# Kernel optimization log

Measured on AMD Instinct MI355X. Metric: run time of the kernel, lower is better.

The kernel has to match this reference:

```python
import jax, jax.numpy as jnp
import numpy as np

N_HEAD = 32
N_KV_HEAD = 8
HEAD_DIM = 64
ROPE_THETA = 10000.0


def apply_rope(x):
    # x: [B, H, T, D], interleaved-pair RoPE (rotary_embedding_torch style)
    B, H, T, D = x.shape
    inv_freq = 1.0 / (ROPE_THETA ** (jnp.arange(0, D, 2, dtype=jnp.float32) / D))  # [D/2]
    ang = jnp.arange(T, dtype=jnp.float32)[:, None] * inv_freq[None, :]  # [T, D/2]
    cos = jnp.cos(ang)[None, None].astype(x.dtype)  # [1,1,T,D/2]
    sin = jnp.sin(ang)[None, None].astype(x.dtype)
    xe = x[..., 0::2]
    xo = x[..., 1::2]
    re = xe * cos - xo * sin
    ro = xo * cos + xe * sin
    return jnp.stack([re, ro], axis=-1).reshape(B, H, T, D)


def setup_inputs() -> dict:
    key = jax.random.key(0)
    ks = jax.random.split(key, 5)
    B, T, C = 2, 2048, 2048
    kv_dim = N_KV_HEAD * HEAD_DIM
    s = 0.02
    return {
        "x": jax.random.normal(ks[0], (B, T, C), jnp.float32),
        "wq": jax.random.normal(ks[1], (C, C), jnp.float32) * s,
        "wk": jax.random.normal(ks[2], (C, kv_dim), jnp.float32) * s,
        "wv": jax.random.normal(ks[3], (C, kv_dim), jnp.float32) * s,
        "wo": jax.random.normal(ks[4], (C, C), jnp.float32) * s,
    }


def reference(x, wq, wk, wv, wo):
    B, T, C = x.shape
    hd = HEAD_DIM
    q = (x @ wq).reshape(B, T, N_HEAD, hd).transpose(0, 2, 1, 3)      # [B,H,T,d]
    k = (x @ wk).reshape(B, T, N_KV_HEAD, hd).transpose(0, 2, 1, 3)   # [B,Hkv,T,d]
    v = (x @ wv).reshape(B, T, N_KV_HEAD, hd).transpose(0, 2, 1, 3)
    q = apply_rope(q)
    k = apply_rope(k)
    rep = N_HEAD // N_KV_HEAD
    k = jnp.repeat(k, rep, axis=1)  # repeat_interleave over head dim
    v = jnp.repeat(v, rep, axis=1)
    att = jnp.einsum('bhqd,bhkd->bhqk', q, k) * (1.0 / np.sqrt(hd))
    causal = jnp.tril(jnp.ones((T, T), dtype=bool))
    att = jnp.where(causal[None, None], att, jnp.finfo(att.dtype).min)
    att = jax.nn.softmax(att, axis=-1)
    y = jnp.einsum('bhqk,bhkd->bhqd', att, v)
    y = y.transpose(0, 2, 1, 3).reshape(B, T, C)
    return y @ wo
```

## Files before the change

kernel.cpp:

```cpp
#include <hip/hip_runtime.h>
#include <hip/hip_bf16.h>
#include <cstdint>
#include <cstddef>


using bf16 = __hip_bfloat16;
using f32x4  = __attribute__((ext_vector_type(4))) float;
using f32x16 = __attribute__((ext_vector_type(16))) float;
using short8 = __attribute__((ext_vector_type(8))) short;
using u32x4  = __attribute__((ext_vector_type(4))) unsigned int;

typedef __attribute__((address_space(1))) const void* gp1_t;
typedef __attribute__((address_space(3))) void*       lp3_t;

#define GLOAD_LDS16(g, l)                                                     \
  __builtin_amdgcn_global_load_lds((gp1_t)(const void*)(g), (lp3_t)(void*)(l), 16, 0, 0)

#define MFMA16(a, b, c) __builtin_amdgcn_mfma_f32_16x16x32_bf16(a, b, c, 0, 0, 0)
#define MFMA32(a, b, c) __builtin_amdgcn_mfma_f32_32x32x16_bf16(a, b, c, 0, 0, 0)

static constexpr int Bd  = 2;
static constexpr int Td  = 2048;
static constexpr int Cd  = 2048;
static constexpr int NH  = 32;
static constexpr int NKV = 8;
static constexpr int HD  = 64;
static constexpr int Md  = Bd * Td;

__device__ inline float bf2f(unsigned short u) {
  union { unsigned int i; float f; } v; v.i = ((unsigned int)u) << 16; return v.f;
}
__device__ inline unsigned short f2bfbits(float f) {
  union { float f; unsigned int u; } v; v.f = f;
  unsigned int r = v.u + 0x7fffu + ((v.u >> 16) & 1u);
  return (unsigned short)(r >> 16);
}
__device__ inline unsigned int pkbf(float a, float b) {
  unsigned int r;
  asm("v_cvt_pk_bf16_f32 %0, %1, %2" : "=v"(r) : "v"(a), "v"(b));
  return r;
}
__device__ inline void plswapf(float& a, float& b) {
  asm("v_permlane32_swap_b32 %0, %1" : "+v"(a), "+v"(b));
}
__device__ inline void plswapu(unsigned int& a, unsigned int& b) {
  asm("v_permlane32_swap_b32 %0, %1" : "+v"(a), "+v"(b));
}
__device__ inline float hmax16(const f32x16& v) {
  float a0 = fmaxf(v[0], v[1]),   a1 = fmaxf(v[2], v[3]);
  float a2 = fmaxf(v[4], v[5]),   a3 = fmaxf(v[6], v[7]);
  float a4 = fmaxf(v[8], v[9]),   a5 = fmaxf(v[10], v[11]);
  float a6 = fmaxf(v[12], v[13]), a7 = fmaxf(v[14], v[15]);
  float b0 = fmaxf(a0, a1), b1 = fmaxf(a2, a3);
  float b2 = fmaxf(a4, a5), b3 = fmaxf(a6, a7);
  return fmaxf(fmaxf(b0, b1), fmaxf(b2, b3));
}
__device__ inline float hsum16(const f32x16& v) {
  float a0 = v[0]+v[1],   a1 = v[2]+v[3],   a2 = v[4]+v[5],   a3 = v[6]+v[7];
  float a4 = v[8]+v[9],   a5 = v[10]+v[11], a6 = v[12]+v[13], a7 = v[14]+v[15];
  float b0 = a0+a1, b1 = a2+a3, b2 = a4+a5, b3 = a6+a7;
  return (b0+b1)+(b2+b3);
}

__global__ __launch_bounds__(256) void prep1_kernel(const float* __restrict__ x,
                                                    const float* __restrict__ wq,
                                                    const float* __restrict__ wk,
                                                    const float* __restrict__ wv,
                                                    bf16* __restrict__ xb,
                                                    bf16* __restrict__ w1) {
  __shared__ float tile[32][33];
  int bid = blockIdx.x, tid = threadIdx.x;
  if (bid < 8192) {
    int i = bid * 256 + tid;
    float4 v = ((const float4*)x)[i];
    ushort4 o;
    o.x = f2bfbits(v.x); o.y = f2bfbits(v.y); o.z = f2bfbits(v.z); o.w = f2bfbits(v.w);
    ((ushort4*)xb)[i] = o;
    return;
  }
  const float* in; bf16* out; int Cc, bx, by;
  if (bid < 12288)      { int l = bid - 8192;  in = wq; out = w1;                        Cc = 2048; bx = l & 63; by = l >> 6; }
  else if (bid < 13312) { int l = bid - 12288; in = wk; out = w1 + (size_t)2048 * 2048;  Cc = 512;  bx = l & 15; by = l >> 4; }
  else                  { int l = bid - 13312; in = wv; out = w1 + (size_t)2560 * 2048;  Cc = 512;  bx = l & 15; by = l >> 4; }
  int tx = tid & 31, ty = tid >> 5;
  int col = bx * 32 + tx;
#pragma unroll
  for (int i = 0; i < 4; ++i) {
    int row = by * 32 + ty + i * 8;
    tile[ty + i * 8][tx] = in[(size_t)row * Cc + col];
  }
  __syncthreads();
#pragma unroll
  for (int i = 0; i < 4; ++i) {
    int orow = bx * 32 + ty + i * 8;
    int ocol = by * 32 + tx;
    out[(size_t)orow * 2048 + ocol] = __float2bfloat16(tile[tx][ty + i * 8]);
  }
}

__global__ __launch_bounds__(256) void transpose_f2b(const float* __restrict__ in,
                                                     bf16* __restrict__ out,
                                                     int R, int Cc) {
  __shared__ float tile[32][33];
  int tx = threadIdx.x & 31, ty = threadIdx.x >> 5;
  int bx = blockIdx.x, by = blockIdx.y;
  int col = bx * 32 + tx;
#pragma unroll
  for (int i = 0; i < 4; ++i) {
    int row = by * 32 + ty + i * 8;
    tile[ty + i * 8][tx] = in[(size_t)row * Cc + col];
  }
  __syncthreads();
#pragma unroll
  for (int i = 0; i < 4; ++i) {
    int orow = bx * 32 + ty + i * 8;
    int ocol = by * 32 + tx;
    out[(size_t)orow * R + ocol] = __float2bfloat16(tile[tx][ty + i * 8]);
  }
}

__global__ __launch_bounds__(512, 2) void gemm_qkv(const bf16* __restrict__ A,
                                                   const bf16* __restrict__ Bt,
                                                   void* __restrict__ Cp,
                                                   int M, int N, int K) {
  __shared__ __align__(16) char lds[114688];
  int tid = threadIdx.x;
  int w = tid >> 6, lane = tid & 63;
  int lr = lane & 15, lg = lane >> 4;
  int m0 = blockIdx.x * 256, n0 = blockIdx.y * 192;
  int wr = w >> 2, wc = w & 3;
  f32x4 acc[8][3] = {};

  size_t Kb = (size_t)K * 2;
  int c8 = lane & 7, r8 = lane >> 3;
  const char* Asrc = (const char*)A + (size_t)(m0 + w * 8 + r8) * Kb + ((c8 ^ r8) << 4);
  const char* Bsrc = (const char*)Bt + (size_t)(n0 + w * 8 + r8) * Kb + ((c8 ^ r8) << 4);
  char* AldsW = lds + w * 1024;
  char* BldsW = lds + 65536 + w * 1024;

#define GSTAGE(kt, bb) do {                                                   \
    _Pragma("unroll")                                                         \
    for (int j = 0; j < 4; ++j)                                               \
      GLOAD_LDS16(Asrc + (size_t)j * 64 * Kb + (size_t)(kt) * 2,              \
                  AldsW + (bb) * 32768 + j * 8192);                           \
    _Pragma("unroll")                                                         \
    for (int j = 0; j < 3; ++j)                                               \
      GLOAD_LDS16(Bsrc + (size_t)j * 64 * Kb + (size_t)(kt) * 2,              \
                  BldsW + (bb) * 24576 + j * 8192);                           \
  } while (0)

  int nkt = K >> 6;
  GSTAGE(0, 0);
  asm volatile("s_waitcnt vmcnt(0)" ::: "memory");
  __builtin_amdgcn_s_barrier();

  for (int t = 0; t < nkt; ++t) {
    int cur = t & 1;
    const char* Ab = lds + cur * 32768;
    const char* Bb = lds + 65536 + cur * 24576;
    short8 af[4][2], bfr[3][2];

    if (t + 1 < nkt) GSTAGE((t + 1) << 6, cur ^ 1);
#pragma unroll
    for (int kk = 0; kk < 2; ++kk) {
      int cb = (((kk << 2) | lg) ^ (lr & 7)) << 4;
#pragma unroll
      for (int f = 0; f < 4; ++f)
        af[f][kk] = *(const short8*)(Ab + (size_t)(wr * 128 + f * 16 + lr) * 128 + cb);
#pragma unroll
      for (int g = 0; g < 3; ++g)
        bfr[g][kk] = *(const short8*)(Bb + (size_t)(wc * 48 + g * 16 + lr) * 128 + cb);
    }
    __builtin_amdgcn_s_barrier();
    asm volatile("s_waitcnt lgkmcnt(0)" ::: "memory");
    __builtin_amdgcn_sched_barrier(0);
    __builtin_amdgcn_s_setprio(1);
#pragma unroll
    for (int f = 0; f < 4; ++f)
#pragma unroll
      for (int g = 0; g < 3; ++g)
#pragma unroll
        for (int kk = 0; kk < 2; ++kk)
          acc[f][g] = MFMA16(af[f][kk], bfr[g][kk], acc[f][g]);
    __builtin_amdgcn_s_setprio(0);
    __builtin_amdgcn_sched_barrier(0);
    __builtin_amdgcn_s_barrier();

#pragma unroll
    for (int kk = 0; kk < 2; ++kk) {
      int cb = (((kk << 2) | lg) ^ (lr & 7)) << 4;
#pragma unroll
      for (int f = 0; f < 4; ++f)
        af[f][kk] = *(const short8*)(Ab + (size_t)(wr * 128 + 64 + f * 16 + lr) * 128 + cb);
    }
    __builtin_amdgcn_s_barrier();
    asm volatile("s_waitcnt lgkmcnt(0)" ::: "memory");
    __builtin_amdgcn_sched_barrier(0);
    __builtin_amdgcn_s_setprio(1);
#pragma unroll
    for (int f = 0; f < 4; ++f)
#pragma unroll
      for (int g = 0; g < 3; ++g)
#pragma unroll
        for (int kk = 0; kk < 2; ++kk)
          acc[4 + f][g] = MFMA16(af[f][kk], bfr[g][kk], acc[4 + f][g]);
    __builtin_amdgcn_s_setprio(0);
    __builtin_amdgcn_sched_barrier(0);
    asm volatile("s_waitcnt vmcnt(0)" ::: "memory");
    __builtin_amdgcn_s_barrier();
  }
#undef GSTAGE

  bf16* Qb  = (bf16*)Cp;
  bf16* Kb2 = Qb + (size_t)Bd * NH * Td * HD;
  bf16* Vtb = Kb2 + (size_t)Bd * NKV * Td * HD;

  int b    = m0 >> 11;
  int col0 = n0 + wc * 48;

  if (col0 >= 2560) {
    int tg = (m0 & 2047) + wr * 128;
    int d0 = col0 - 2560;
    char* tb = lds + w * 14336;
#pragma unroll
    for (int i = 0; i < 8; ++i)
#pragma unroll
      for (int j = 0; j < 3; ++j)
#pragma unroll
        for (int r = 0; r < 4; r += 2) {
          int dl = j * 16 + lr;
          int tt = i * 16 + lg * 4 + r;
          unsigned int pk = pkbf(acc[i][j][r], acc[i][j][r + 1]);
          *(unsigned int*)(tb + (((size_t)dl * 256 + tt * 2) ^ ((dl & 7) << 4))) = pk;
        }
    asm volatile("s_waitcnt lgkmcnt(0)" ::: "memory");
    __builtin_amdgcn_sched_barrier(0);
#pragma unroll
    for (int p = 0; p < 12; ++p) {
      int c  = p * 64 + lane;
      int dl = c >> 4;
      int tc = c & 15;
      int dg = d0 + dl;
      int h  = dg >> 6, dd = dg & 63;
      u32x4 v = *(const u32x4*)(tb + (((size_t)dl * 256 + tc * 16) ^ ((dl & 7) << 4)));
      *(u32x4*)((char*)Vtb + ((((size_t)b * NKV + h) * 64 + dd) * Td + tg) * 2 + tc * 16) = v;
    }
    return;
  }

  const float RC  = -0.41524101186092029f;
  const float QSC = 0.18033688011112042f;
  int odd = lane & 1;
#pragma unroll
  for (int j = 0; j < 3; ++j) {
    int ncol = col0 + j * 16 + lr;
    int d  = ncol & 63;
    float inv = __builtin_amdgcn_exp2f((float)(d >> 1) * RC);
#pragma unroll
    for (int i = 0; i < 8; ++i) {
#pragma unroll
      for (int r = 0; r < 4; ++r) {
        int mrow = m0 + wr * 128 + i * 16 + lg * 4 + r;
        int t = mrow & 2047;
        float raw = acc[i][j][r];
        float p = __shfl_xor(raw, 1);
        float rev = (float)t * inv * 0.15915494309189535f;
        rev = rev - floorf(rev);
        float s = __builtin_amdgcn_sinf(rev);
        float c = __builtin_amdgcn_cosf(rev);
        float res = odd ? (raw * c + p * s) : (raw * c - p * s);
        if (ncol < 2048) {
          int h = ncol >> 6;
          Qb[(((size_t)b * NH + h) * Td + t) * HD + d] = __float2bfloat16(res * QSC);
        } else if (ncol < 2560) {
          int h = (ncol - 2048) >> 6;
          Kb2[(((size_t)b * NKV + h) * Td + t) * HD + d] = __float2bfloat16(res);
        } else {
          int dg = ncol - 2560;
          int h = dg >> 6, dd = dg & 63;
          Vtb[(((size_t)b * NKV + h) * 64 + dd) * Td + t] = __float2bfloat16(raw);
        }
      }
    }
  }
}

__global__ __launch_bounds__(256, 2) void gemm_out(const bf16* __restrict__ A,
                                                   const bf16* __restrict__ Bt,
                                                   float* __restrict__ Cp,
                                                   int M, int N, int K) {
  __shared__ __align__(16) bf16 Al[2][128 * 64];
  __shared__ __align__(16) bf16 Bl[2][128 * 64];
  int tid = threadIdx.x;
  int w = tid >> 6, lane = tid & 63;
  int lr = lane & 15, lg = lane >> 4;
  int m0 = blockIdx.x * 128, n0 = blockIdx.y * 128;
  int wr = w >> 1, wc = w & 1;
  f32x4 acc[4][4] = {};

  size_t Kb = (size_t)K * 2;
  int c8 = lane & 7, r8 = lane >> 3;
  const char* Asrc = (const char*)A + (size_t)(m0 + w * 8 + r8) * Kb + ((c8 ^ r8) << 4);
  const char* Bsrc = (const char*)Bt + (size_t)(n0 + w * 8 + r8) * Kb + ((c8 ^ r8) << 4);

#define GSTAGE(kt, bb) do {                                                   \
    char* ald = (char*)&Al[bb][0] + w * 1024;                                 \
    char* bld = (char*)&Bl[bb][0] + w * 1024;                                 \
    _Pragma("unroll")                                                         \
    for (int j = 0; j < 4; ++j) {                                             \
      GLOAD_LDS16(Asrc + (size_t)j * 32 * Kb + (size_t)(kt) * 2, ald + j * 4096); \
      GLOAD_LDS16(Bsrc + (size_t)j * 32 * Kb + (size_t)(kt) * 2, bld + j * 4096); \
    }                                                                         \
  } while (0)

  int nkt = K >> 6;
  GSTAGE(0, 0);
  asm volatile("s_waitcnt vmcnt(0)" ::: "memory");
  __builtin_amdgcn_s_barrier();
  __builtin_amdgcn_sched_barrier(0);

  for (int t = 0; t < nkt; ++t) {
    int cur = t & 1;
    if (t + 1 < nkt) {
      GSTAGE((t + 1) << 6, cur ^ 1);
      asm volatile("s_waitcnt vmcnt(8)" ::: "memory");
    } else {
      asm volatile("s_waitcnt vmcnt(0)" ::: "memory");
    }
    __builtin_amdgcn_s_barrier();
    __builtin_amdgcn_sched_barrier(0);
    const char* Ab = (const char*)&Al[cur][0];
    const char* Bb = (const char*)&Bl[cur][0];
    __builtin_amdgcn_s_setprio(1);
#pragma unroll
    for (int kk = 0; kk < 2; ++kk) {
      short8 af[4], bfr[4];
#pragma unroll
      for (int f = 0; f < 4; ++f) {
        int ra = wr * 64 + f * 16 + lr;
        int rb = wc * 64 + f * 16 + lr;
        int cb = (((kk << 2) | lg) ^ (lr & 7)) << 4;
        af[f]  = *(const short8*)(Ab + (size_t)ra * 128 + cb);
        bfr[f] = *(const short8*)(Bb + (size_t)rb * 128 + cb);
      }
#pragma unroll
      for (int i = 0; i < 4; ++i)
#pragma unroll
        for (int j = 0; j < 4; ++j)
          acc[i][j] = MFMA16(af[i], bfr[j], acc[i][j]);
    }
    __builtin_amdgcn_s_setprio(0);
    asm volatile("s_waitcnt lgkmcnt(0)" ::: "memory");
    __builtin_amdgcn_sched_barrier(0);
    __builtin_amdgcn_s_barrier();
  }
#undef GSTAGE

#pragma unroll
  for (int i = 0; i < 4; ++i)
#pragma unroll
    for (int j = 0; j < 4; ++j)
#pragma unroll
      for (int r = 0; r < 4; ++r) {
        int mrow = m0 + wr * 64 + i * 16 + lg * 4 + r;
        int ncol = n0 + wc * 64 + j * 16 + lr;
        Cp[(size_t)mrow * N + ncol] = acc[i][j][r];
      }
}

__global__ __launch_bounds__(512, 4) void attn_kernel(const bf16* __restrict__ Q,
                                                      const bf16* __restrict__ K,
                                                      const bf16* __restrict__ Vt,
                                                      bf16* __restrict__ Y) {
  __shared__ __align__(16) char lds[2 * 16384];
  int tid = threadIdx.x, w = tid >> 6, lane = tid & 63;
  int lq = lane & 31;
  int H  = lane >> 5;
  int qb = 7 - (int)blockIdx.y;
  int bh = blockIdx.x;
  int b = bh >> 5, h = bh & 31, kvh = h >> 2;
  int q0w = qb * 256 + w * 32;
  int qg  = q0w + lq;
  int tmax = qb * 4 + (w >> 1);
  int Nt   = qb * 4 + 4;

  const bf16* Qp = Q + (((size_t)b * NH + h) * Td) * HD;
  const char* Kg = (const char*)(K + (((size_t)b * NKV + kvh) * Td) * HD);
  const char* Vg = (const char*)(Vt + (((size_t)b * NKV + kvh) * HD) * Td);

  short8 qf[4];
#pragma unroll
  for (int ck = 0; ck < 4; ++ck)
    qf[ck] = *(const short8*)(Qp + (size_t)qg * HD + ck * 16 + H * 8);

  int srow   = lane >> 3;
  int scol16 = ((lane & 7) ^ srow) << 4;
  const char* Ksrc0 = Kg + (size_t)(w * 8 + srow) * 128 + scol16;
  const char* Vsrc0 = Vg + (size_t)(w * 8 + srow) * 4096 + scol16;
  char* KldsW[2] = { lds + w * 1024,          lds + 16384 + w * 1024 };
  char* VldsW[2] = { lds + 8192 + w * 1024,   lds + 24576 + w * 1024 };

#define STAGE_KV(tt, bb) do {                                                 \
    GLOAD_LDS16(Ksrc0 + (size_t)(tt) * 64 * 128, KldsW[bb]);                  \
    GLOAD_LDS16(Vsrc0 + (size_t)(tt) * 128,      VldsW[bb]);                  \
  } while (0)

  f32x16 acc0 = {}, acc1 = {};
  float m = -3e38f, l = 0.0f;
  int swz = (lq & 7) << 4;
  int rb0 = lq * 128, rb1 = (32 + lq) * 128;

  STAGE_KV(0, 0);
  asm volatile("s_waitcnt vmcnt(0)" ::: "memory");
  __syncthreads();

  for (int t = 0; t < Nt; ++t) {
    int cur = t & 1;
    if (t + 1 < Nt) STAGE_KV(t + 1, cur ^ 1);
    if (t <= tmax) {
      const char* Kl = lds + cur * 16384;
      const char* Vl = Kl + 8192;
      f32x16 s0 = {}, s1 = {};
      __builtin_amdgcn_s_setprio(1);
#pragma unroll
      for (int ck = 0; ck < 4; ++ck) {
        int c = (H * 16 + ck * 32) ^ swz;
        short8 kf0 = *(const short8*)(Kl + rb0 + c);
        short8 kf1 = *(const short8*)(Kl + rb1 + c);
        s0 = MFMA32(kf0, qf[ck], s0);
        s1 = MFMA32(kf1, qf[ck], s1);
      }
      __builtin_amdgcn_s_setprio(0);
      if (t == tmax) {
        int kvb = t * 64;
#pragma unroll
        for (int rr = 0; rr < 16; ++rr) {
          int krel = (rr & 3) + 8 * (rr >> 2) + 4 * H;
          if (kvb + krel > qg)      s0[rr] = -3e38f;
          if (kvb + 32 + krel > qg) s1[rr] = -3e38f;
        }
      }
      float mx = fmaxf(hmax16(s0), hmax16(s1));
      {
        float mb = mx;
        asm("" : "+v"(mb));
        plswapf(mx, mb);
        mx = fmaxf(mx, mb);
      }
      if (__any(mx > m + 8.0f)) {
        float mn = fmaxf(m, mx);
        float al = __builtin_amdgcn_exp2f(m - mn);
        m = mn;
        l *= al;
#pragma unroll
        for (int rr = 0; rr < 16; ++rr) { acc0[rr] *= al; acc1[rr] *= al; }
      }
#pragma unroll
      for (int rr = 0; rr < 16; ++rr) {
        s0[rr] = __builtin_amdgcn_exp2f(s0[rr] - m);
        s1[rr] = __builtin_amdgcn_exp2f(s1[rr] - m);
      }
      float ps = hsum16(s0) + hsum16(s1);
      {
        float pb = ps;
        asm("" : "+v"(pb));
        plswapf(ps, pb);
        ps += pb;
      }
      l += ps;
      short8 pf[4];
#pragma unroll
      for (int tt = 0; tt < 2; ++tt) {
        const f32x16& sv = tt ? s1 : s0;
#pragma unroll
        for (int a2 = 0; a2 < 2; ++a2) {
          unsigned int A0 = pkbf(sv[8*a2 + 0], sv[8*a2 + 1]);
          unsigned int A1 = pkbf(sv[8*a2 + 2], sv[8*a2 + 3]);
          unsigned int B0 = pkbf(sv[8*a2 + 4], sv[8*a2 + 5]);
          unsigned int B1 = pkbf(sv[8*a2 + 6], sv[8*a2 + 7]);
          plswapu(A0, B0);
          plswapu(A1, B1);
          u32x4 t4;
          t4[0] = A0; t4[1] = A1; t4[2] = B0; t4[3] = B1;
          pf[2*tt + a2] = __builtin_bit_cast(short8, t4);
        }
      }
      __builtin_amdgcn_s_setprio(1);
#pragma unroll
      for (int ks = 0; ks < 4; ++ks) {
        int c = (H * 16 + ks * 32) ^ swz;
        short8 vf0 = *(const short8*)(Vl + rb0 + c);
        short8 vf1 = *(const short8*)(Vl + rb1 + c);
        acc0 = MFMA32(vf0, pf[ks], acc0);
        acc1 = MFMA32(vf1, pf[ks], acc1);
      }
      __builtin_amdgcn_s_setprio(0);
    }
    asm volatile("s_waitcnt vmcnt(0)" ::: "memory");
    __syncthreads();
  }
#undef STAGE_KV

  float rn = 1.0f / l;
  bf16* Yp = Y + ((size_t)b * Td + qg) * Cd + h * HD;
#pragma unroll
  for (int rr = 0; rr < 16; rr += 2) {
    int d = (rr & 3) + 8 * (rr >> 2) + 4 * H;
    unsigned int w0 = pkbf(acc0[rr] * rn, acc0[rr + 1] * rn);
    unsigned int w1 = pkbf(acc1[rr] * rn, acc1[rr + 1] * rn);
    *(unsigned int*)(Yp + d)      = w0;
    *(unsigned int*)(Yp + 32 + d) = w1;
  }
}

extern "C" void kernel_launch(void* const* d_in, const int* in_sizes, int n_in,
                              void* d_out, int out_size, void* d_ws, size_t ws_size,
                              hipStream_t stream) {
  const float* x  = (const float*)d_in[0];
  const float* wq = (const float*)d_in[1];
  const float* wk = (const float*)d_in[2];
  const float* wv = (const float*)d_in[3];
  const float* wo = (const float*)d_in[4];

  char* ws = (char*)d_ws;
  const size_t o_xb = 0;
  const size_t o_w1 = o_xb + (size_t)Md * Cd * 2;
  const size_t o_Q  = o_w1 + (size_t)3072 * Cd * 2;
  const size_t o_K  = o_Q + (size_t)Bd * NH * Td * HD * 2;
  const size_t o_V  = o_K + (size_t)Bd * NKV * Td * HD * 2;

  bf16* xb  = (bf16*)(ws + o_xb);
  bf16* w1  = (bf16*)(ws + o_w1);
  bf16* Qb  = (bf16*)(ws + o_Q);
  bf16* Kb  = (bf16*)(ws + o_K);
  bf16* Vtb = (bf16*)(ws + o_V);
  bf16* yb  = xb;

  prep1_kernel<<<dim3(14336), dim3(256), 0, stream>>>(x, wq, wk, wv, xb, w1);
  gemm_qkv<<<dim3(Md / 256, 3072 / 192), dim3(512), 0, stream>>>(xb, w1, Qb, Md, 3072, Cd);
  transpose_f2b<<<dim3(Cd / 32, Cd / 32), dim3(256), 0, stream>>>(wo, w1, Cd, Cd);
  attn_kernel<<<dim3(Bd * NH, 8), dim3(512), 0, stream>>>(Qb, Kb, Vtb, yb);
  gemm_out<<<dim3(Md / 128, Cd / 128), dim3(256), 0, stream>>>(yb, w1, (float*)d_out, Md, Cd, Cd);
}
```

Baseline: 185.4 us.

## Retile output GEMM to 256x128 with 8 waves and fold wo transpose into prep

The output projection GEMM now uses 512-thread blocks computing 256x128 tiles. Each wave handles a 128x32 slab, split into two half-phases with separate LDS reads and barriers, and the next K-tile's global-to-LDS loads are issued before the MFMAs. Separately, the wo transpose/convert moves into the prep1 kernel, writing to its own workspace region when the workspace is large enough, which removes one kernel launch and lets wo be converted before the QKV GEMM. In exchange the GEMM uses 96KB of LDS per block, adds more barriers, and launches half as many blocks, which may reduce occupancy.

```diff
diff --git a/kernel.cpp b/kernel.cpp
--- a/kernel.cpp
+++ b/kernel.cpp
@@ -66,8 +66,10 @@
                                                     const float* __restrict__ wq,
                                                     const float* __restrict__ wk,
                                                     const float* __restrict__ wv,
+                                                    const float* __restrict__ wo,
                                                     bf16* __restrict__ xb,
-                                                    bf16* __restrict__ w1) {
+                                                    bf16* __restrict__ w1,
+                                                    bf16* __restrict__ woT) {
   __shared__ float tile[32][33];
   int bid = blockIdx.x, tid = threadIdx.x;
   if (bid < 8192) {
@@ -81,7 +83,8 @@
   const float* in; bf16* out; int Cc, bx, by;
   if (bid < 12288)      { int l = bid - 8192;  in = wq; out = w1;                        Cc = 2048; bx = l & 63; by = l >> 6; }
   else if (bid < 13312) { int l = bid - 12288; in = wk; out = w1 + (size_t)2048 * 2048;  Cc = 512;  bx = l & 15; by = l >> 4; }
-  else                  { int l = bid - 13312; in = wv; out = w1 + (size_t)2560 * 2048;  Cc = 512;  bx = l & 15; by = l >> 4; }
+  else if (bid < 14336) { int l = bid - 13312; in = wv; out = w1 + (size_t)2560 * 2048;  Cc = 512;  bx = l & 15; by = l >> 4; }
+  else                  { int l = bid - 14336; in = wo; out = woT;                       Cc = 2048; bx = l & 63; by = l >> 6; }
   int tx = tid & 31, ty = tid >> 5;
   int col = bx * 32 + tx;
 #pragma unroll
@@ -285,85 +288,106 @@
   }
 }
 
-__global__ __launch_bounds__(256, 2) void gemm_out(const bf16* __restrict__ A,
+__global__ __launch_bounds__(512, 2) void gemm_out(const bf16* __restrict__ A,
                                                    const bf16* __restrict__ Bt,
                                                    float* __restrict__ Cp,
                                                    int M, int N, int K) {
-  __shared__ __align__(16) bf16 Al[2][128 * 64];
-  __shared__ __align__(16) bf16 Bl[2][128 * 64];
+  __shared__ __align__(16) char lds[98304];
   int tid = threadIdx.x;
   int w = tid >> 6, lane = tid & 63;
   int lr = lane & 15, lg = lane >> 4;
-  int m0 = blockIdx.x * 128, n0 = blockIdx.y * 128;
-  int wr = w >> 1, wc = w & 1;
-  f32x4 acc[4][4] = {};
+  int m0 = blockIdx.x * 256, n0 = blockIdx.y * 128;
+  int wr = w >> 2, wc = w & 3;
+  f32x4 acc[8][2] = {};
 
   size_t Kb = (size_t)K * 2;
   int c8 = lane & 7, r8 = lane >> 3;
   const char* Asrc = (const char*)A + (size_t)(m0 + w * 8 + r8) * Kb + ((c8 ^ r8) << 4);
   const char* Bsrc = (const char*)Bt + (size_t)(n0 + w * 8 + r8) * Kb + ((c8 ^ r8) << 4);
+  char* AldsW = lds + w * 1024;
+  char* BldsW = lds + 65536 + w * 1024;
 
 #define GSTAGE(kt, bb) do {                                                   \
-    char* ald = (char*)&Al[bb][0] + w * 1024;                                 \
-    char* bld = (char*)&Bl[bb][0] + w * 1024;                                 \
     _Pragma("unroll")                                                         \
-    for (int j = 0; j < 4; ++j) {                                             \
-      GLOAD_LDS16(Asrc + (size_t)j * 32 * Kb + (size_t)(kt) * 2, ald + j * 4096); \
-      GLOAD_LDS16(Bsrc + (size_t)j * 32 * Kb + (size_t)(kt) * 2, bld + j * 4096); \
-    }                                                                         \
+    for (int j = 0; j < 4; ++j)                                               \
+      GLOAD_LDS16(Asrc + (size_t)j * 64 * Kb + (size_t)(kt) * 2,              \
+                  AldsW + (bb) * 32768 + j * 8192);                           \
+    _Pragma("unroll")                                                         \
+    for (int j = 0; j < 2; ++j)                                               \
+      GLOAD_LDS16(Bsrc + (size_t)j * 64 * Kb + (size_t)(kt) * 2,              \
+                  BldsW + (bb) * 16384 + j * 8192);                           \
   } while (0)
 
   int nkt = K >> 6;
   GSTAGE(0, 0);
   asm volatile("s_waitcnt vmcnt(0)" ::: "memory");
   __builtin_amdgcn_s_barrier();
-  __builtin_amdgcn_sched_barrier(0);
 
   for (int t = 0; t < nkt; ++t) {
     int cur = t & 1;
-    if (t + 1 < nkt) {
-      GSTAGE((t + 1) << 6, cur ^ 1);
-      asm volatile("s_waitcnt vmcnt(8)" ::: "memory");
-    } else {
-      asm volatile("s_waitcnt vmcnt(0)" ::: "memory");
-    }
-    __builtin_amdgcn_s_barrier();
-    __builtin_amdgcn_sched_barrier(0);
-    const char* Ab = (const char*)&Al[cur][0];
-    const char* Bb = (const char*)&Bl[cur][0];
+    const char* Ab = lds + cur * 32768;
+    const char* Bb = lds + 65536 + cur * 16384;
+    short8 af[4][2], bfr[2][2];
+
+    if (t + 1 < nkt) GSTAGE((t + 1) << 6, cur ^ 1);
+#pragma unroll
+    for (int kk = 0; kk < 2; ++kk) {
+      int cb = (((kk << 2) | lg) ^ (lr & 7)) << 4;
+#pragma unroll
+      for (int f = 0; f < 4; ++f)
+        af[f][kk] = *(const short8*)(Ab + (size_t)(wr * 128 + f * 16 + lr) * 128 + cb);
+#pragma unroll
+      for (int g = 0; g < 2; ++g)
+        bfr[g][kk] = *(const short8*)(Bb + (size_t)(wc * 32 + g * 16 + lr) * 128 + cb);
+    }
+    __builtin_amdgcn_s_barrier();
+    asm volatile("s_waitcnt lgkmcnt(0)" ::: "memory");
+    __builtin_amdgcn_sched_barrier(0);
     __builtin_amdgcn_s_setprio(1);
 #pragma unroll
+    for (int f = 0; f < 4; ++f)
+#pragma unroll
+      for (int g = 0; g < 2; ++g)
+#pragma unroll
+        for (int kk = 0; kk < 2; ++kk)
+          acc[f][g] = MFMA16(af[f][kk], bfr[g][kk], acc[f][g]);
+    __builtin_amdgcn_s_setprio(0);
+    __builtin_amdgcn_sched_barrier(0);
+    __builtin_amdgcn_s_barrier();
+
+#pragma unroll
     for (int kk = 0; kk < 2; ++kk) {
-      short8 af[4], bfr[4];
-#pragma unroll
-      for (int f = 0; f < 4; ++f) {
-        int ra = wr * 64 + f * 16 + lr;
-        int rb = wc * 64 + f * 16 + lr;
-        int cb = (((kk << 2) | lg) ^ (lr & 7)) << 4;
-        af[f]  = *(const short8*)(Ab + (size_t)ra * 128 + cb);
-        bfr[f] = *(const short8*)(Bb + (size_t)rb * 128 + cb);
-      }
-#pragma unroll
-      for (int i = 0; i < 4; ++i)
-#pragma unroll
-        for (int j = 0; j < 4; ++j)
-          acc[i][j] = MFMA16(af[i], bfr[j], acc[i][j]);
-    }
+      int cb = (((kk << 2) | lg) ^ (lr & 7)) << 4;
+#pragma unroll
+      for (int f = 0; f < 4; ++f)
+        af[f][kk] = *(const short8*)(Ab + (size_t)(wr * 128 + 64 + f * 16 + lr) * 128 + cb);
+    }
+    __builtin_amdgcn_s_barrier();
+    asm volatile("s_waitcnt lgkmcnt(0)" ::: "memory");
+    __builtin_amdgcn_sched_barrier(0);
+    __builtin_amdgcn_s_setprio(1);
+#pragma unroll
+    for (int f = 0; f < 4; ++f)
+#pragma unroll
+      for (int g = 0; g < 2; ++g)
+#pragma unroll
+        for (int kk = 0; kk < 2; ++kk)
+          acc[4 + f][g] = MFMA16(af[f][kk], bfr[g][kk], acc[4 + f][g]);
     __builtin_amdgcn_s_setprio(0);
-    asm volatile("s_waitcnt lgkmcnt(0)" ::: "memory");
-    __builtin_amdgcn_sched_barrier(0);
+    __builtin_amdgcn_sched_barrier(0);
+    asm volatile("s_waitcnt vmcnt(0)" ::: "memory");
     __builtin_amdgcn_s_barrier();
   }
 #undef GSTAGE
 
 #pragma unroll
-  for (int i = 0; i < 4; ++i)
-#pragma unroll
-    for (int j = 0; j < 4; ++j)
+  for (int i = 0; i < 8; ++i)
+#pragma unroll
+    for (int j = 0; j < 2; ++j)
 #pragma unroll
       for (int r = 0; r < 4; ++r) {
-        int mrow = m0 + wr * 64 + i * 16 + lg * 4 + r;
-        int ncol = n0 + wc * 64 + j * 16 + lr;
+        int mrow = m0 + wr * 128 + i * 16 + lg * 4 + r;
+        int ncol = n0 + wc * 32 + j * 16 + lr;
         Cp[(size_t)mrow * N + ncol] = acc[i][j][r];
       }
 }
@@ -523,11 +547,13 @@
   const float* wo = (const float*)d_in[4];
 
   char* ws = (char*)d_ws;
-  const size_t o_xb = 0;
-  const size_t o_w1 = o_xb + (size_t)Md * Cd * 2;
-  const size_t o_Q  = o_w1 + (size_t)3072 * Cd * 2;
-  const size_t o_K  = o_Q + (size_t)Bd * NH * Td * HD * 2;
-  const size_t o_V  = o_K + (size_t)Bd * NKV * Td * HD * 2;
+  const size_t o_xb  = 0;
+  const size_t o_w1  = o_xb + (size_t)Md * Cd * 2;
+  const size_t o_Q   = o_w1 + (size_t)3072 * Cd * 2;
+  const size_t o_K   = o_Q + (size_t)Bd * NH * Td * HD * 2;
+  const size_t o_V   = o_K + (size_t)Bd * NKV * Td * HD * 2;
+  const size_t o_woT = o_V + (size_t)Bd * NKV * HD * Td * 2;
+  const size_t need  = o_woT + (size_t)Cd * Cd * 2;
 
   bf16* xb  = (bf16*)(ws + o_xb);
   bf16* w1  = (bf16*)(ws + o_w1);
@@ -536,9 +562,14 @@
   bf16* Vtb = (bf16*)(ws + o_V);
   bf16* yb  = xb;
 
-  prep1_kernel<<<dim3(14336), dim3(256), 0, stream>>>(x, wq, wk, wv, xb, w1);
+  bool fused = (ws_size >= need);
+  bf16* woT = fused ? (bf16*)(ws + o_woT) : w1;
+
+  prep1_kernel<<<dim3(fused ? 18432 : 14336), dim3(256), 0, stream>>>(
+      x, wq, wk, wv, wo, xb, w1, woT);
   gemm_qkv<<<dim3(Md / 256, 3072 / 192), dim3(512), 0, stream>>>(xb, w1, Qb, Md, 3072, Cd);
-  transpose_f2b<<<dim3(Cd / 32, Cd / 32), dim3(256), 0, stream>>>(wo, w1, Cd, Cd);
+  if (!fused)
+    transpose_f2b<<<dim3(Cd / 32, Cd / 32), dim3(256), 0, stream>>>(wo, w1, Cd, Cd);
   attn_kernel<<<dim3(Bd * NH, 8), dim3(512), 0, stream>>>(Qb, Kb, Vtb, yb);
-  gemm_out<<<dim3(Md / 128, Cd / 128), dim3(256), 0, stream>>>(yb, w1, (float*)d_out, Md, Cd, Cd);
-}
+  gemm_out<<<dim3(Md / 256, Cd / 128), dim3(512), 0, stream>>>(yb, woT, (float*)d_out, Md, Cd, Cd);
+}
```

After: 183.4 us. Within noise of the previous version (-1.1%).
